# Performance work log

Hardware: AMD Instinct MI355X
Metric: run time of the kernel (lower is better)

## Reference

```python
import jax, jax.numpy as jnp
import numpy as np

NEG_SLOPE = 0.2


def gat_conv(h, src, dst, n_dst, W_src, W_dst, attn_l, attn_r, bias):
    # h: [N_src, F_in]; edges src->dst; dst nodes are a prefix of src nodes.
    H, D = attn_l.shape
    z_src = (h @ W_src).reshape(h.shape[0], H, D)          # [N_src, H, D]
    z_dst = (h[:n_dst] @ W_dst).reshape(n_dst, H, D)       # [N_dst, H, D]
    el = jnp.einsum('nhd,hd->nh', z_src, attn_l)           # [N_src, H]
    er = jnp.einsum('nhd,hd->nh', z_dst, attn_r)           # [N_dst, H]
    e = jax.nn.leaky_relu(el[src] + er[dst], NEG_SLOPE)    # [E, H]
    # numerically stable edge softmax over incoming edges of each dst node
    m = jax.ops.segment_max(e, dst, num_segments=n_dst)    # [N_dst, H]
    w = jnp.exp(e - m[dst])                                # [E, H]
    s = jax.ops.segment_sum(w, dst, num_segments=n_dst)    # [N_dst, H]
    alpha = w / s[dst]                                     # [E, H]
    msg = alpha[:, :, None] * z_src[src]                   # [E, H, D]
    out = jax.ops.segment_sum(msg, dst, num_segments=n_dst)
    return out + bias                                      # [N_dst, H, D]


def setup_inputs() -> dict:
    key = jax.random.key(0)
    ks = jax.random.split(key, 16)
    IN, HID, HEADS, NCLS = 256, 64, 4, 47
    N_SRC0, N_DST0, E0 = 200000, 50000, 500000
    N_DST1, E1 = 10000, 100000
    sc0 = 0.1
    inp = {
        'x': jax.random.normal(ks[0], (N_SRC0, IN), jnp.float32),
        'src0': jax.random.randint(ks[1], (E0,), 0, N_SRC0, jnp.int32),
        'dst0': jax.random.randint(ks[2], (E0,), 0, N_DST0, jnp.int32),
        'src1': jax.random.randint(ks[3], (E1,), 0, N_DST0, jnp.int32),
        'dst1': jax.random.randint(ks[4], (E1,), 0, N_DST1, jnp.int32),
        'num_dst0': N_DST0,
        'num_dst1': N_DST1,
        'W0_src': jax.random.normal(ks[5], (IN, HEADS * HID), jnp.float32) * sc0,
        'W0_dst': jax.random.normal(ks[6], (IN, HEADS * HID), jnp.float32) * sc0,
        'attn_l0': jax.random.normal(ks[7], (HEADS, HID), jnp.float32) * sc0,
        'attn_r0': jax.random.normal(ks[8], (HEADS, HID), jnp.float32) * sc0,
        'bias0': jnp.zeros((HEADS, HID), jnp.float32),
        'W1_src': jax.random.normal(ks[9], (HEADS * HID, HEADS * NCLS), jnp.float32) * sc0,
        'W1_dst': jax.random.normal(ks[10], (HEADS * HID, HEADS * NCLS), jnp.float32) * sc0,
        'attn_l1': jax.random.normal(ks[11], (HEADS, NCLS), jnp.float32) * sc0,
        'attn_r1': jax.random.normal(ks[12], (HEADS, NCLS), jnp.float32) * sc0,
        'bias1': jnp.zeros((HEADS, NCLS), jnp.float32),
    }
    return inp


def reference(x, src0, dst0, src1, dst1, num_dst0, num_dst1,
              W0_src, W0_dst, attn_l0, attn_r0, bias0,
              W1_src, W1_dst, attn_l1, attn_r1, bias1):
    # layer 0: GATConv + relu activation, flatten heads
    h = gat_conv(x, src0, dst0, num_dst0, W0_src, W0_dst, attn_l0, attn_r0, bias0)
    h = jax.nn.relu(h).reshape(num_dst0, -1)               # [N_dst0, H*HID]
    # layer 1: GATConv, no activation
    h = gat_conv(h, src1, dst1, num_dst1, W1_src, W1_dst, attn_l1, attn_r1, bias1)
    h = h.mean(axis=1)                                     # mean over heads -> [N_dst1, n_classes]
    return jax.nn.log_softmax(h, axis=-1)
```

## Files before the change

### kernel.cpp

```cpp
#include <hip/hip_runtime.h>
#include <math.h>

typedef _Float16 half8 __attribute__((ext_vector_type(8)));
typedef _Float16 half4 __attribute__((ext_vector_type(4)));
typedef float f32x16 __attribute__((ext_vector_type(16)));

constexpr int IN    = 256;
constexpr int NCLS  = 47;
constexpr int HD1   = 188;
constexpr float NEG_SLOPE = 0.2f;
constexpr int ND0 = 50000, ND1 = 10000;

static __device__ __forceinline__ float leaky(float x) {
    return x >= 0.f ? x : NEG_SLOPE * x;
}

__device__ __forceinline__ void gload16(const void* g, void* l) {
    __builtin_amdgcn_global_load_lds((const __attribute__((address_space(1))) void*)g,
                                     (__attribute__((address_space(3))) void*)l, 16, 0, 0);
}

__global__ __launch_bounds__(256) void prep_k(
        const float* __restrict__ W0s, const float* __restrict__ W1s,
        const float* __restrict__ W0d, const float* __restrict__ W1d,
        const float* __restrict__ ar0, const float* __restrict__ al1,
        const float* __restrict__ ar1,
        _Float16* __restrict__ B0t, _Float16* __restrict__ B1t,
        float* __restrict__ vr0T, float* __restrict__ vl1T, float* __restrict__ vr1T) {
    int b = blockIdx.x, t = threadIdx.x;
    if (b < 256) {
        int id = b * 256 + t;
        int n = id >> 8, k = id & 255;
        B0t[n * 256 + k] = (_Float16)W0s[(size_t)k * 256 + n];
    } else if (b < 448) {
        int id = (b - 256) * 256 + t;
        int n = id >> 8, k = id & 255;
        B1t[n * 256 + k] = (n < HD1) ? (_Float16)W1s[(size_t)k * HD1 + n] : (_Float16)0.f;
    } else if (b == 448) {
        for (int i = t; i < 1024; i += 256) {
            int h = i >> 8, k = i & 255;
            float s = 0.f;
            for (int d = 0; d < 64; ++d)
                s += W0d[(size_t)k * 256 + h * 64 + d] * ar0[h * 64 + d];
            vr0T[h * 256 + k] = s;
        }
    } else if (b == 449) {
        for (int i = t; i < 1024; i += 256) {
            int h = i >> 8, k = i & 255;
            float s = 0.f;
            for (int d = 0; d < NCLS; ++d)
                s += W1s[(size_t)k * HD1 + h * NCLS + d] * al1[h * NCLS + d];
            vl1T[h * 256 + k] = s;
        }
    } else {
        for (int i = t; i < 1024; i += 256) {
            int h = i >> 8, k = i & 255;
            float s = 0.f;
            for (int d = 0; d < NCLS; ++d)
                s += W1d[(size_t)k * HD1 + h * NCLS + d] * ar1[h * NCLS + d];
            vr1T[h * 256 + k] = s;
        }
    }
}

template <bool AHALF, int NWC, bool FEL>
__global__ __launch_bounds__(512, 4) void gemmk(const void* __restrict__ Av,
        const _Float16* __restrict__ Bt, _Float16* __restrict__ Z,
        const float* __restrict__ al, float* __restrict__ el, int M, int ntiles) {
    constexpr int ABYTES = AHALF ? 16 * 1040 : 32 * 1040;
    __shared__ __align__(16) char As[2][ABYTES];
    __shared__ float elp[2][8][32];
    __shared__ float alds[256];
    const int t = threadIdx.x, l = t & 63, w = t >> 6;
    const int l31 = l & 31, hi = l >> 5;
    const int G = gridDim.x;

    if (FEL && t < 256) alds[t] = al[t];

    half8 wk[16];
    {
        int wc = (w < NWC) ? w * 32 + l31 : 0;
        const _Float16* bp = Bt + (size_t)wc * 256 + hi * 8;
#pragma unroll
        for (int ks = 0; ks < 16; ++ks) wk[ks] = *(const half8*)(bp + ks * 16);
    }

    auto stage = [&](int buf, int tile) {
        if constexpr (AHALF) {
#pragma unroll
            for (int i = 0; i < 2; ++i) {
                int pr = w * 2 + i;
                int row = tile * 32 + pr * 2 + hi;
                if (row >= M) row = M - 1;
                gload16((const _Float16*)Av + (size_t)row * 256 + l31 * 8,
                        As[buf] + pr * 1040);
            }
        } else {
#pragma unroll
            for (int i = 0; i < 4; ++i) {
                int r = w * 4 + i;
                int row = tile * 32 + r;
                if (row >= M) row = M - 1;
                gload16((const float*)Av + (size_t)row * 256 + l * 4,
                        As[buf] + r * 1040);
            }
        }
    };

    int tile0 = blockIdx.x;
    stage(0, tile0);
    asm volatile("s_waitcnt vmcnt(0)" ::: "memory");
    __syncthreads();

    int buf = 0;
    for (int tile = tile0; tile < ntiles; tile += G) {
        int nxt = tile + G;
        if (nxt < ntiles) stage(buf ^ 1, nxt);

        if (w < NWC) {
            f32x16 acc;
#pragma unroll
            for (int e = 0; e < 16; ++e) acc[e] = 0.f;
#pragma unroll
            for (int ks = 0; ks < 16; ++ks) {
                half8 bf;
                if constexpr (AHALF) {
                    bf = *(const half8*)(As[buf] + (l31 >> 1) * 1040 + (l31 & 1) * 512
                                         + ks * 32 + hi * 16);
                } else {
                    const char* ab = As[buf] + l31 * 1040 + ks * 64 + hi * 32;
                    float4 f0 = *(const float4*)ab;
                    float4 f1 = *(const float4*)(ab + 16);
                    bf[0] = (_Float16)f0.x; bf[1] = (_Float16)f0.y;
                    bf[2] = (_Float16)f0.z; bf[3] = (_Float16)f0.w;
                    bf[4] = (_Float16)f1.x; bf[5] = (_Float16)f1.y;
                    bf[6] = (_Float16)f1.z; bf[7] = (_Float16)f1.w;
                }
                acc = __builtin_amdgcn_mfma_f32_32x32x16_f16(wk[ks], bf, acc, 0, 0, 0);
            }
            int xrow = tile * 32 + l31;
            if (xrow < M) {
#pragma unroll
                for (int g = 0; g < 4; ++g) {
                    half4 hv;
                    hv[0] = (_Float16)acc[g * 4 + 0]; hv[1] = (_Float16)acc[g * 4 + 1];
                    hv[2] = (_Float16)acc[g * 4 + 2]; hv[3] = (_Float16)acc[g * 4 + 3];
                    *(half4*)(Z + (size_t)xrow * (NWC * 32) + w * 32 + g * 8 + hi * 4) = hv;
                }
            }
            if constexpr (FEL) {
                float s = 0.f;
#pragma unroll
                for (int q = 0; q < 16; ++q)
                    s += acc[q] * alds[w * 32 + (q & 3) + 8 * (q >> 2) + 4 * hi];
                s += __shfl_xor(s, 32);
                if (hi == 0) elp[buf][w][l31] = s;
            }
        }
        asm volatile("s_waitcnt vmcnt(0)" ::: "memory");
        __syncthreads();
        if constexpr (FEL) {
            if (w < 4 && hi == 0) {
                int xrow = tile * 32 + l31;
                if (xrow < M)
                    el[(size_t)xrow * 4 + w] =
                        elp[buf][2 * w][l31] + elp[buf][2 * w + 1][l31];
            }
        }
        buf ^= 1;
    }
}

__global__ __launch_bounds__(256) void gemv_er_f32(const float* __restrict__ A,
        const float* __restrict__ vrT, float* __restrict__ er, int M) {
    int wv = threadIdx.x >> 6, lane = threadIdx.x & 63;
    int row = blockIdx.x * 4 + wv;
    if (row >= M) return;
    float4 xa = *(const float4*)(A + (size_t)row * IN + lane * 4);
    float s[4];
#pragma unroll
    for (int h = 0; h < 4; ++h) {
        float4 v = *(const float4*)(vrT + h * IN + lane * 4);
        s[h] = xa.x * v.x + xa.y * v.y + xa.z * v.z + xa.w * v.w;
    }
#pragma unroll
    for (int off = 32; off; off >>= 1)
#pragma unroll
        for (int h = 0; h < 4; ++h) s[h] += __shfl_xor(s[h], off);
    if (lane == 0) *(float4*)(er + (size_t)row * 4) = make_float4(s[0], s[1], s[2], s[3]);
}

__global__ __launch_bounds__(256) void gemv_lr_f16(const _Float16* __restrict__ A,
        const float* __restrict__ vlT, const float* __restrict__ vrT,
        float* __restrict__ el, float* __restrict__ er, int M, int Mr) {
    int wv = threadIdx.x >> 6, lane = threadIdx.x & 63;
    int row = blockIdx.x * 4 + wv;
    if (row >= M) return;
    half4 ah = *(const half4*)(A + (size_t)row * IN + lane * 4);
    float a0 = (float)ah[0], a1 = (float)ah[1], a2 = (float)ah[2], a3 = (float)ah[3];
    float sl[4], sr[4];
#pragma unroll
    for (int h = 0; h < 4; ++h) {
        float4 v = *(const float4*)(vlT + h * IN + lane * 4);
        sl[h] = a0 * v.x + a1 * v.y + a2 * v.z + a3 * v.w;
        float4 u = *(const float4*)(vrT + h * IN + lane * 4);
        sr[h] = a0 * u.x + a1 * u.y + a2 * u.z + a3 * u.w;
    }
#pragma unroll
    for (int off = 32; off; off >>= 1)
#pragma unroll
        for (int h = 0; h < 4; ++h) {
            sl[h] += __shfl_xor(sl[h], off);
            sr[h] += __shfl_xor(sr[h], off);
        }
    if (lane == 0) {
        *(float4*)(el + (size_t)row * 4) = make_float4(sl[0], sl[1], sl[2], sl[3]);
        if (row < Mr)
            *(float4*)(er + (size_t)row * 4) = make_float4(sr[0], sr[1], sr[2], sr[3]);
    }
}

__global__ void hist2_k(const int* __restrict__ dst0, int E0,
                        const int* __restrict__ dst1, int E1, int* __restrict__ counts) {
    int i = blockIdx.x * blockDim.x + threadIdx.x;
    if (i < E0) atomicAdd(&counts[dst0[i]], 1);
    else if (i < E0 + E1) atomicAdd(&counts[ND0 + dst1[i - E0]], 1);
}

__global__ __launch_bounds__(256) void scan1_k(const int* __restrict__ counts, int n,
                                               int* __restrict__ part) {
    __shared__ int ws[4];
    int i = blockIdx.x * 256 + threadIdx.x;
    int lane = threadIdx.x & 63, wv = threadIdx.x >> 6;
    int s = (i < n) ? counts[i] : 0;
#pragma unroll
    for (int off = 32; off; off >>= 1) s += __shfl_xor(s, off);
    if (lane == 0) ws[wv] = s;
    __syncthreads();
    if (threadIdx.x == 0) part[blockIdx.x] = ws[0] + ws[1] + ws[2] + ws[3];
}

__global__ __launch_bounds__(256) void scan2_k(int* __restrict__ part, int nb) {
    __shared__ int ws[4];
    int tid = threadIdx.x, lane = tid & 63, wv = tid >> 6;
    int v = (tid < nb) ? part[tid] : 0;
    int x = v;
#pragma unroll
    for (int off = 1; off < 64; off <<= 1) {
        int u = __shfl_up(x, off);
        if (lane >= off) x += u;
    }
    if (lane == 63) ws[wv] = x;
    __syncthreads();
    int base = 0;
    for (int k = 0; k < wv; ++k) base += ws[k];
    if (tid < nb) part[tid] = base + x - v;
}

__global__ __launch_bounds__(256) void scan3_k(const int* __restrict__ counts, int n,
        const int* __restrict__ part, int* __restrict__ offsets, int* __restrict__ cursor) {
    __shared__ int ws[4];
    int i = blockIdx.x * 256 + threadIdx.x;
    int lane = threadIdx.x & 63, wv = threadIdx.x >> 6;
    int v = (i < n) ? counts[i] : 0;
    int x = v;
#pragma unroll
    for (int off = 1; off < 64; off <<= 1) {
        int u = __shfl_up(x, off);
        if (lane >= off) x += u;
    }
    if (lane == 63) ws[wv] = x;
    __syncthreads();
    int base = part[blockIdx.x];
    for (int k = 0; k < wv; ++k) base += ws[k];
    int off_ = base + x - v;
    if (i < n) { offsets[i] = off_; cursor[i] = off_; }
    if (i == n - 1) offsets[n] = off_ + v;
}

__global__ void scatter2_k(const int* __restrict__ src0, const int* __restrict__ dst0, int E0,
                           const int* __restrict__ src1, const int* __restrict__ dst1, int E1,
                           int* __restrict__ cursor, int* __restrict__ ssrc) {
    int i = blockIdx.x * blockDim.x + threadIdx.x;
    if (i < E0) {
        int p = atomicAdd(&cursor[dst0[i]], 1);
        ssrc[p] = src0[i];
    } else if (i < E0 + E1) {
        int j = i - E0;
        int p = atomicAdd(&cursor[ND0 + dst1[j]], 1);
        ssrc[p] = src1[j];
    }
}

__global__ __launch_bounds__(256) void agg_l0(const int* __restrict__ ssrc,
        const int* __restrict__ offs, const float* __restrict__ el,
        const float* __restrict__ er, const _Float16* __restrict__ z,
        const float* __restrict__ bias, _Float16* __restrict__ h, int nd) {
    int wv = threadIdx.x >> 6, lane = threadIdx.x & 63;
    int d = blockIdx.x * 4 + wv;
    if (d >= nd) return;
    int head = lane >> 4;
    int beg = offs[d], end = offs[d + 1];
    float erh = er[(size_t)d * 4 + head];
    float ax = 0, ay = 0, az = 0, aw = 0, ssum = 0;
    for (int j0 = beg; j0 < end; j0 += 64) {
        int nn = min(64, end - j0);
        int myidx = (lane < nn) ? ssrc[j0 + lane] : 0;
        int j = 0;
        for (; j + 4 <= nn; j += 4) {
            int s0 = __shfl(myidx, j),     s1 = __shfl(myidx, j + 1);
            int s2 = __shfl(myidx, j + 2), s3 = __shfl(myidx, j + 3);
            float e0 = el[(size_t)s0 * 4 + head], e1 = el[(size_t)s1 * 4 + head];
            float e2 = el[(size_t)s2 * 4 + head], e3 = el[(size_t)s3 * 4 + head];
            half4 zv0 = *(const half4*)(z + (size_t)s0 * 256 + lane * 4);
            half4 zv1 = *(const half4*)(z + (size_t)s1 * 256 + lane * 4);
            half4 zv2 = *(const half4*)(z + (size_t)s2 * 256 + lane * 4);
            half4 zv3 = *(const half4*)(z + (size_t)s3 * 256 + lane * 4);
            float w0 = __expf(leaky(e0 + erh)), w1 = __expf(leaky(e1 + erh));
            float w2 = __expf(leaky(e2 + erh)), w3 = __expf(leaky(e3 + erh));
            ssum += (w0 + w1) + (w2 + w3);
            ax += w0 * (float)zv0[0] + w1 * (float)zv1[0] + w2 * (float)zv2[0] + w3 * (float)zv3[0];
            ay += w0 * (float)zv0[1] + w1 * (float)zv1[1] + w2 * (float)zv2[1] + w3 * (float)zv3[1];
            az += w0 * (float)zv0[2] + w1 * (float)zv1[2] + w2 * (float)zv2[2] + w3 * (float)zv3[2];
            aw += w0 * (float)zv0[3] + w1 * (float)zv1[3] + w2 * (float)zv2[3] + w3 * (float)zv3[3];
        }
        for (; j < nn; ++j) {
            int s = __shfl(myidx, j);
            float e = el[(size_t)s * 4 + head] + erh;
            float wgt = __expf(leaky(e));
            ssum += wgt;
            half4 zv = *(const half4*)(z + (size_t)s * 256 + lane * 4);
            ax += wgt * (float)zv[0]; ay += wgt * (float)zv[1];
            az += wgt * (float)zv[2]; aw += wgt * (float)zv[3];
        }
    }
    float inv = ssum > 0.f ? 1.f / ssum : 0.f;
    const float* b = bias + lane * 4;
    half4 o;
    o[0] = (_Float16)fmaxf(ax * inv + b[0], 0.f);
    o[1] = (_Float16)fmaxf(ay * inv + b[1], 0.f);
    o[2] = (_Float16)fmaxf(az * inv + b[2], 0.f);
    o[3] = (_Float16)fmaxf(aw * inv + b[3], 0.f);
    *(half4*)(h + (size_t)d * 256 + lane * 4) = o;
}

__global__ __launch_bounds__(256) void agg_l1f(const int* __restrict__ ssrc,
        const int* __restrict__ offs, const float* __restrict__ el,
        const float* __restrict__ er, const _Float16* __restrict__ z,
        const float* __restrict__ bias, float* __restrict__ y, int nd) {
    __shared__ float ro[4][192];
    int wv = threadIdx.x >> 6, lane = threadIdx.x & 63;
    int d = blockIdx.x * 4 + wv;
    if (d >= nd) return;
    int beg = offs[ND0 + d], end = offs[ND0 + d + 1];
    float4 er4 = *(const float4*)(er + (size_t)d * 4);
    const int f0 = lane, f1 = lane + 64, f2 = lane + 128;
    const int h0 = f0 / NCLS, h1 = f1 / NCLS;
    const bool has2 = f2 < HD1;
    const int h2 = has2 ? f2 / NCLS : 3;
    float a0 = 0, a1 = 0, a2 = 0;
    float s0 = 0, s1 = 0, s2 = 0, s3 = 0;
    for (int j0 = beg; j0 < end; j0 += 64) {
        int nn = min(64, end - j0);
        int myidx = (lane < nn) ? ssrc[j0 + lane] : 0;
        int j = 0;
        for (; j + 2 <= nn; j += 2) {
            int sa_ = __shfl(myidx, j), sb_ = __shfl(myidx, j + 1);
            float4 ea = *(const float4*)(el + (size_t)sa_ * 4);
            float4 eb = *(const float4*)(el + (size_t)sb_ * 4);
            const _Float16* za = z + (size_t)sa_ * 192;
            const _Float16* zb = z + (size_t)sb_ * 192;
            float za0 = (float)za[f0], za1 = (float)za[f1], za2 = has2 ? (float)za[f2] : 0.f;
            float zb0 = (float)zb[f0], zb1 = (float)zb[f1], zb2 = has2 ? (float)zb[f2] : 0.f;
            float wa0 = __expf(leaky(ea.x + er4.x)), wa1 = __expf(leaky(ea.y + er4.y));
            float wa2 = __expf(leaky(ea.z + er4.z)), wa3 = __expf(leaky(ea.w + er4.w));
            float wb0 = __expf(leaky(eb.x + er4.x)), wb1 = __expf(leaky(eb.y + er4.y));
            float wb2 = __expf(leaky(eb.z + er4.z)), wb3 = __expf(leaky(eb.w + er4.w));
            s0 += wa0 + wb0; s1 += wa1 + wb1; s2 += wa2 + wb2; s3 += wa3 + wb3;
            a0 += (h0 == 0 ? wa0 : h0 == 1 ? wa1 : h0 == 2 ? wa2 : wa3) * za0
                + (h0 == 0 ? wb0 : h0 == 1 ? wb1 : h0 == 2 ? wb2 : wb3) * zb0;
            a1 += (h1 == 0 ? wa0 : h1 == 1 ? wa1 : h1 == 2 ? wa2 : wa3) * za1
                + (h1 == 0 ? wb0 : h1 == 1 ? wb1 : h1 == 2 ? wb2 : wb3) * zb1;
            if (has2)
                a2 += (h2 == 0 ? wa0 : h2 == 1 ? wa1 : h2 == 2 ? wa2 : wa3) * za2
                    + (h2 == 0 ? wb0 : h2 == 1 ? wb1 : h2 == 2 ? wb2 : wb3) * zb2;
        }
        for (; j < nn; ++j) {
            int s = __shfl(myidx, j);
            float4 e4 = *(const float4*)(el + (size_t)s * 4);
            float w0 = __expf(leaky(e4.x + er4.x));
            float w1 = __expf(leaky(e4.y + er4.y));
            float w2 = __expf(leaky(e4.z + er4.z));
            float w3 = __expf(leaky(e4.w + er4.w));
            s0 += w0; s1 += w1; s2 += w2; s3 += w3;
            const _Float16* zr = z + (size_t)s * 192;
            a0 += (h0 == 0 ? w0 : h0 == 1 ? w1 : h0 == 2 ? w2 : w3) * (float)zr[f0];
            a1 += (h1 == 0 ? w0 : h1 == 1 ? w1 : h1 == 2 ? w2 : w3) * (float)zr[f1];
            if (has2) a2 += (h2 == 0 ? w0 : h2 == 1 ? w1 : h2 == 2 ? w2 : w3) * (float)zr[f2];
        }
    }
    float sa = h0 == 0 ? s0 : h0 == 1 ? s1 : h0 == 2 ? s2 : s3;
    float sb = h1 == 0 ? s0 : h1 == 1 ? s1 : h1 == 2 ? s2 : s3;
    float sc = h2 == 0 ? s0 : h2 == 1 ? s1 : h2 == 2 ? s2 : s3;
    ro[wv][f0] = a0 * (sa > 0.f ? 1.f / sa : 0.f) + bias[f0];
    ro[wv][f1] = a1 * (sb > 0.f ? 1.f / sb : 0.f) + bias[f1];
    if (has2) ro[wv][f2] = a2 * (sc > 0.f ? 1.f / sc : 0.f) + bias[f2];
    asm volatile("s_waitcnt lgkmcnt(0)" ::: "memory");
    __builtin_amdgcn_sched_barrier(0);
    float vv = 0.f, v = -INFINITY;
    if (lane < NCLS) {
        vv = 0.25f * (ro[wv][lane] + ro[wv][lane + NCLS] +
                      ro[wv][lane + 2 * NCLS] + ro[wv][lane + 3 * NCLS]);
        v = vv;
    }
    float mx = v;
#pragma unroll
    for (int off = 32; off; off >>= 1) mx = fmaxf(mx, __shfl_xor(mx, off));
    float pp = (lane < NCLS) ? __expf(vv - mx) : 0.f;
    float sum = pp;
#pragma unroll
    for (int off = 32; off; off >>= 1) sum += __shfl_xor(sum, off);
    if (lane < NCLS) y[(size_t)d * NCLS + lane] = vv - mx - logf(sum);
}

extern "C" void kernel_launch(void* const* d_in, const int* in_sizes, int n_in,
                              void* d_out, int out_size, void* d_ws, size_t ws_size,
                              hipStream_t stream) {
    const float* x    = (const float*)d_in[0];
    const int*   src0 = (const int*)d_in[1];
    const int*   dst0 = (const int*)d_in[2];
    const int*   src1 = (const int*)d_in[3];
    const int*   dst1 = (const int*)d_in[4];
    const float* W0s  = (const float*)d_in[7];
    const float* W0d  = (const float*)d_in[8];
    const float* al0  = (const float*)d_in[9];
    const float* ar0  = (const float*)d_in[10];
    const float* b0   = (const float*)d_in[11];
    const float* W1s  = (const float*)d_in[12];
    const float* W1d  = (const float*)d_in[13];
    const float* al1  = (const float*)d_in[14];
    const float* ar1  = (const float*)d_in[15];
    const float* b1   = (const float*)d_in[16];
    const int E0 = in_sizes[1], E1 = in_sizes[3];
    const int NS0 = in_sizes[0] / IN;

    char* p = (char*)d_ws;
    auto take = [&](size_t bytes) {
        char* r = p;
        p += (bytes + 255) & ~(size_t)255;
        return r;
    };
    _Float16* z0   = (_Float16*)take((size_t)NS0 * 256 * 2);
    _Float16* h    = (_Float16*)take((size_t)ND0 * 256 * 2);
    _Float16* z1   = (_Float16*)take((size_t)ND0 * 192 * 2);
    float*    el0  = (float*)take((size_t)NS0 * 4 * 4);
    float*    er0  = (float*)take((size_t)ND0 * 4 * 4);
    float*    el1  = (float*)take((size_t)ND0 * 4 * 4);
    float*    er1  = (float*)take((size_t)ND1 * 4 * 4);
    _Float16* B0t  = (_Float16*)take((size_t)256 * 256 * 2);
    _Float16* B1t  = (_Float16*)take((size_t)192 * 256 * 2);
    float*    vr0T = (float*)take(4 * 256 * 4);
    float*    vl1T = (float*)take(4 * 256 * 4);
    float*    vr1T = (float*)take(4 * 256 * 4);
    const int NDT = ND0 + ND1;
    int* counts = (int*)take((size_t)NDT * 4);
    int* offs   = (int*)take((size_t)(NDT + 1) * 4);
    int* cur    = (int*)take((size_t)NDT * 4);
    int* ss     = (int*)take((size_t)(E0 + E1) * 4);
    int* part   = (int*)take(256 * 4);

    const int NB = (NDT + 255) / 256;
    const int NT0 = (NS0 + 31) / 32, NT1 = (ND0 + 31) / 32;
    const int G0 = NT0 < 512 ? NT0 : 512, G1 = NT1 < 512 ? NT1 : 512;

    hipMemsetAsync(counts, 0, (size_t)NDT * 4, stream);

    prep_k<<<451, 256, 0, stream>>>(W0s, W1s, W0d, W1d, ar0, al1, ar1,
                                    B0t, B1t, vr0T, vl1T, vr1T);
    hist2_k<<<(E0 + E1 + 255) / 256, 256, 0, stream>>>(dst0, E0, dst1, E1, counts);
    scan1_k<<<NB, 256, 0, stream>>>(counts, NDT, part);
    scan2_k<<<1, 256, 0, stream>>>(part, NB);
    scan3_k<<<NB, 256, 0, stream>>>(counts, NDT, part, offs, cur);
    scatter2_k<<<(E0 + E1 + 255) / 256, 256, 0, stream>>>(src0, dst0, E0, src1, dst1, E1,
                                                          cur, ss);

    gemmk<false, 8, true><<<G0, 512, 0, stream>>>(
        (const void*)x, B0t, z0, al0, el0, NS0, NT0);
    gemv_er_f32<<<(ND0 + 3) / 4, 256, 0, stream>>>(x, vr0T, er0, ND0);
    agg_l0<<<(ND0 + 3) / 4, 256, 0, stream>>>(ss, offs, el0, er0, z0, b0, h, ND0);

    gemmk<true, 6, false><<<G1, 512, 0, stream>>>(
        (const void*)h, B1t, z1, nullptr, nullptr, ND0, NT1);
    gemv_lr_f16<<<(ND0 + 3) / 4, 256, 0, stream>>>(h, vl1T, vr1T, el1, er1, ND0, ND1);
    agg_l1f<<<(ND1 + 3) / 4, 256, 0, stream>>>(ss, offs, el1, er1, z1, b1,
                                               (float*)d_out, ND1);
}
```

Baseline: 321.9 us.

## Stage GEMM A tiles through registers as fp16 with swizzled LDS layout

Replaces the direct global-to-LDS loads with register prefetch of the next tile. The fp32 input is converted to fp16 before it is written into a smaller, XOR-swizzled LDS buffer, so MFMA operand reads become single conflict-free half8 loads. The el epilogue is restructured to run after one barrier per iteration instead of two, with a final flush after the loop. This cuts LDS footprint and conversion work in the inner loop, at the cost of extra registers to hold the prefetched payload.

```diff
diff --git a/kernel.cpp b/kernel.cpp
--- a/kernel.cpp
+++ b/kernel.cpp
@@ -13,11 +13,6 @@
 
 static __device__ __forceinline__ float leaky(float x) {
     return x >= 0.f ? x : NEG_SLOPE * x;
-}
-
-__device__ __forceinline__ void gload16(const void* g, void* l) {
-    __builtin_amdgcn_global_load_lds((const __attribute__((address_space(1))) void*)g,
-                                     (__attribute__((address_space(3))) void*)l, 16, 0, 0);
 }
 
 __global__ __launch_bounds__(256) void prep_k(
@@ -67,8 +62,7 @@
 __global__ __launch_bounds__(512, 4) void gemmk(const void* __restrict__ Av,
         const _Float16* __restrict__ Bt, _Float16* __restrict__ Z,
         const float* __restrict__ al, float* __restrict__ el, int M, int ntiles) {
-    constexpr int ABYTES = AHALF ? 16 * 1040 : 32 * 1040;
-    __shared__ __align__(16) char As[2][ABYTES];
+    __shared__ __align__(16) char As[2][32 * 576];
     __shared__ float elp[2][8][32];
     __shared__ float alds[256];
     const int t = threadIdx.x, l = t & 63, w = t >> 6;
@@ -85,57 +79,59 @@
         for (int ks = 0; ks < 16; ++ks) wk[ks] = *(const half8*)(bp + ks * 16);
     }
 
-    auto stage = [&](int buf, int tile) {
-        if constexpr (AHALF) {
-#pragma unroll
-            for (int i = 0; i < 2; ++i) {
-                int pr = w * 2 + i;
-                int row = tile * 32 + pr * 2 + hi;
-                if (row >= M) row = M - 1;
-                gload16((const _Float16*)Av + (size_t)row * 256 + l31 * 8,
-                        As[buf] + pr * 1040);
+    float4 payf[4];
+    half4  payh[4];
+
+    auto issue = [&](int tile) {
+#pragma unroll
+        for (int i = 0; i < 4; ++i) {
+            int row = tile * 32 + w * 4 + i;
+            if (row >= M) row = M - 1;
+            if constexpr (AHALF)
+                payh[i] = *(const half4*)((const _Float16*)Av + (size_t)row * 256 + l * 4);
+            else
+                payf[i] = *(const float4*)((const float*)Av + (size_t)row * 256 + l * 4);
+        }
+        __builtin_amdgcn_sched_barrier(0);
+    };
+
+    auto write_lds = [&](int b) {
+#pragma unroll
+        for (int i = 0; i < 4; ++i) {
+            int rr = w * 4 + i;
+            half4 hv;
+            if constexpr (AHALF) {
+                hv = payh[i];
+            } else {
+                hv[0] = (_Float16)payf[i].x; hv[1] = (_Float16)payf[i].y;
+                hv[2] = (_Float16)payf[i].z; hv[3] = (_Float16)payf[i].w;
             }
-        } else {
-#pragma unroll
-            for (int i = 0; i < 4; ++i) {
-                int r = w * 4 + i;
-                int row = tile * 32 + r;
-                if (row >= M) row = M - 1;
-                gload16((const float*)Av + (size_t)row * 256 + l * 4,
-                        As[buf] + r * 1040);
+            *(half4*)(As[b] + rr * 576 + ((((l >> 1) ^ rr) & 31) << 4) + (l & 1) * 8) = hv;
+        }
+    };
+
+    int tile0 = blockIdx.x;
+    issue(tile0);
+    int b = 0, prev = -1;
+    for (int tile = tile0; tile < ntiles; tile += G) {
+        write_lds(b);
+        if (tile + G < ntiles) issue(tile + G);
+        __syncthreads();
+        if constexpr (FEL) {
+            if (prev >= 0 && w < 4 && hi == 0) {
+                int xr = prev * 32 + l31;
+                if (xr < M)
+                    el[(size_t)xr * 4 + w] = elp[b ^ 1][2 * w][l31] + elp[b ^ 1][2 * w + 1][l31];
             }
         }
-    };
-
-    int tile0 = blockIdx.x;
-    stage(0, tile0);
-    asm volatile("s_waitcnt vmcnt(0)" ::: "memory");
-    __syncthreads();
-
-    int buf = 0;
-    for (int tile = tile0; tile < ntiles; tile += G) {
-        int nxt = tile + G;
-        if (nxt < ntiles) stage(buf ^ 1, nxt);
-
         if (w < NWC) {
             f32x16 acc;
 #pragma unroll
             for (int e = 0; e < 16; ++e) acc[e] = 0.f;
 #pragma unroll
             for (int ks = 0; ks < 16; ++ks) {
-                half8 bf;
-                if constexpr (AHALF) {
-                    bf = *(const half8*)(As[buf] + (l31 >> 1) * 1040 + (l31 & 1) * 512
-                                         + ks * 32 + hi * 16);
-                } else {
-                    const char* ab = As[buf] + l31 * 1040 + ks * 64 + hi * 32;
-                    float4 f0 = *(const float4*)ab;
-                    float4 f1 = *(const float4*)(ab + 16);
-                    bf[0] = (_Float16)f0.x; bf[1] = (_Float16)f0.y;
-                    bf[2] = (_Float16)f0.z; bf[3] = (_Float16)f0.w;
-                    bf[4] = (_Float16)f1.x; bf[5] = (_Float16)f1.y;
-                    bf[6] = (_Float16)f1.z; bf[7] = (_Float16)f1.w;
-                }
+                const char* pa = As[b] + l31 * 576 + ((((ks * 2 + hi) ^ l31) & 31) << 4);
+                half8 bf = *(const half8*)pa;
                 acc = __builtin_amdgcn_mfma_f32_32x32x16_f16(wk[ks], bf, acc, 0, 0, 0);
             }
             int xrow = tile * 32 + l31;
@@ -154,20 +150,19 @@
                 for (int q = 0; q < 16; ++q)
                     s += acc[q] * alds[w * 32 + (q & 3) + 8 * (q >> 2) + 4 * hi];
                 s += __shfl_xor(s, 32);
-                if (hi == 0) elp[buf][w][l31] = s;
+                if (hi == 0) elp[b][w][l31] = s;
             }
         }
-        asm volatile("s_waitcnt vmcnt(0)" ::: "memory");
+        prev = tile;
+        b ^= 1;
+    }
+    if constexpr (FEL) {
         __syncthreads();
-        if constexpr (FEL) {
-            if (w < 4 && hi == 0) {
-                int xrow = tile * 32 + l31;
-                if (xrow < M)
-                    el[(size_t)xrow * 4 + w] =
-                        elp[buf][2 * w][l31] + elp[buf][2 * w + 1][l31];
-            }
-        }
-        buf ^= 1;
+        if (prev >= 0 && w < 4 && hi == 0) {
+            int xr = prev * 32 + l31;
+            if (xr < M)
+                el[(size_t)xr * 4 + w] = elp[b ^ 1][2 * w][l31] + elp[b ^ 1][2 * w + 1][l31];
+        }
     }
 }
 
```

Result: slower. 328.5 us (+2.1%).

## Pre-convert x to fp16 with fused el/er GEMV and 4-stage swizzled GEMM pipeline

Applied to the files above, without the earlier changes.

A new cvt_lr kernel reads x once, writes an fp16 copy, and computes el0 and er0 through precomputed W0s·attn_l and W0d·attn_r vectors. This replaces the el epilogue inside the GEMM and the separate er GEMV. The GEMM is rewritten as gemmd: fp16 input only, a 4-deep LDS ring buffer with a partial vmcnt wait, and XOR-swizzled LDS addressing in place of padded rows. The trade-off is an extra fp16 write and read of x (about 100MB of traffic) in exchange for a simpler, deeper-pipelined MFMA loop with half the A-tile staging bytes.

```diff
diff --git a/kernel.cpp b/kernel.cpp
--- a/kernel.cpp
+++ b/kernel.cpp
@@ -23,10 +23,11 @@
 __global__ __launch_bounds__(256) void prep_k(
         const float* __restrict__ W0s, const float* __restrict__ W1s,
         const float* __restrict__ W0d, const float* __restrict__ W1d,
-        const float* __restrict__ ar0, const float* __restrict__ al1,
-        const float* __restrict__ ar1,
+        const float* __restrict__ al0, const float* __restrict__ ar0,
+        const float* __restrict__ al1, const float* __restrict__ ar1,
         _Float16* __restrict__ B0t, _Float16* __restrict__ B1t,
-        float* __restrict__ vr0T, float* __restrict__ vl1T, float* __restrict__ vr1T) {
+        float* __restrict__ vl0T, float* __restrict__ vr0T,
+        float* __restrict__ vl1T, float* __restrict__ vr1T) {
     int b = blockIdx.x, t = threadIdx.x;
     if (b < 256) {
         int id = b * 256 + t;
@@ -48,6 +49,14 @@
         for (int i = t; i < 1024; i += 256) {
             int h = i >> 8, k = i & 255;
             float s = 0.f;
+            for (int d = 0; d < 64; ++d)
+                s += W0s[(size_t)k * 256 + h * 64 + d] * al0[h * 64 + d];
+            vl0T[h * 256 + k] = s;
+        }
+    } else if (b == 450) {
+        for (int i = t; i < 1024; i += 256) {
+            int h = i >> 8, k = i & 255;
+            float s = 0.f;
             for (int d = 0; d < NCLS; ++d)
                 s += W1s[(size_t)k * HD1 + h * NCLS + d] * al1[h * NCLS + d];
             vl1T[h * 256 + k] = s;
@@ -63,19 +72,49 @@
     }
 }
 
-template <bool AHALF, int NWC, bool FEL>
-__global__ __launch_bounds__(512, 4) void gemmk(const void* __restrict__ Av,
-        const _Float16* __restrict__ Bt, _Float16* __restrict__ Z,
-        const float* __restrict__ al, float* __restrict__ el, int M, int ntiles) {
-    constexpr int ABYTES = AHALF ? 16 * 1040 : 32 * 1040;
-    __shared__ __align__(16) char As[2][ABYTES];
-    __shared__ float elp[2][8][32];
-    __shared__ float alds[256];
+__global__ __launch_bounds__(256) void cvt_lr(const float* __restrict__ x,
+        const float* __restrict__ vlT, const float* __restrict__ vrT,
+        _Float16* __restrict__ xh, float* __restrict__ el, float* __restrict__ er,
+        int M, int Mr) {
+    int wv = threadIdx.x >> 6, lane = threadIdx.x & 63;
+    int row = blockIdx.x * 4 + wv;
+    if (row >= M) return;
+    float4 xa = *(const float4*)(x + (size_t)row * IN + lane * 4);
+    half4 hv;
+    hv[0] = (_Float16)xa.x; hv[1] = (_Float16)xa.y;
+    hv[2] = (_Float16)xa.z; hv[3] = (_Float16)xa.w;
+    *(half4*)(xh + (size_t)row * IN + lane * 4) = hv;
+    float sl[4], sr[4];
+    bool do_r = row < Mr;
+#pragma unroll
+    for (int h = 0; h < 4; ++h) {
+        float4 v = *(const float4*)(vlT + h * IN + lane * 4);
+        sl[h] = xa.x * v.x + xa.y * v.y + xa.z * v.z + xa.w * v.w;
+        float4 u = *(const float4*)(vrT + h * IN + lane * 4);
+        sr[h] = xa.x * u.x + xa.y * u.y + xa.z * u.z + xa.w * u.w;
+    }
+#pragma unroll
+    for (int off = 32; off; off >>= 1)
+#pragma unroll
+        for (int h = 0; h < 4; ++h) {
+            sl[h] += __shfl_xor(sl[h], off);
+            sr[h] += __shfl_xor(sr[h], off);
+        }
+    if (lane == 0) {
+        *(float4*)(el + (size_t)row * 4) = make_float4(sl[0], sl[1], sl[2], sl[3]);
+        if (do_r)
+            *(float4*)(er + (size_t)row * 4) = make_float4(sr[0], sr[1], sr[2], sr[3]);
+    }
+}
+
+template <int NWC>
+__global__ __launch_bounds__(512, 4) void gemmd(const _Float16* __restrict__ Ah,
+        const _Float16* __restrict__ Bt, _Float16* __restrict__ Z, int M, int ntiles) {
+    __shared__ __align__(16) char As[4][16384];
     const int t = threadIdx.x, l = t & 63, w = t >> 6;
     const int l31 = l & 31, hi = l >> 5;
     const int G = gridDim.x;
-
-    if (FEL && t < 256) alds[t] = al[t];
+    const int tile0 = blockIdx.x;
 
     half8 wk[16];
     {
@@ -85,60 +124,38 @@
         for (int ks = 0; ks < 16; ++ks) wk[ks] = *(const half8*)(bp + ks * 16);
     }
 
-    auto stage = [&](int buf, int tile) {
-        if constexpr (AHALF) {
-#pragma unroll
-            for (int i = 0; i < 2; ++i) {
-                int pr = w * 2 + i;
-                int row = tile * 32 + pr * 2 + hi;
-                if (row >= M) row = M - 1;
-                gload16((const _Float16*)Av + (size_t)row * 256 + l31 * 8,
-                        As[buf] + pr * 1040);
-            }
-        } else {
-#pragma unroll
-            for (int i = 0; i < 4; ++i) {
-                int r = w * 4 + i;
-                int row = tile * 32 + r;
-                if (row >= M) row = M - 1;
-                gload16((const float*)Av + (size_t)row * 256 + l * 4,
-                        As[buf] + r * 1040);
-            }
+    auto stage = [&](int it) {
+        int tile = tile0 + it * G;
+        if (tile >= ntiles) return;
+        char* dst = As[it & 3];
+#pragma unroll
+        for (int i = 0; i < 2; ++i) {
+            int c = i * 512 + t;
+            int r = c >> 5, s = c & 31;
+            int row = tile * 32 + r; if (row >= M) row = M - 1;
+            gload16(Ah + (size_t)row * 256 + ((s ^ r) << 3), dst + c * 16);
         }
     };
 
-    int tile0 = blockIdx.x;
-    stage(0, tile0);
-    asm volatile("s_waitcnt vmcnt(0)" ::: "memory");
-    __syncthreads();
-
-    int buf = 0;
-    for (int tile = tile0; tile < ntiles; tile += G) {
-        int nxt = tile + G;
-        if (nxt < ntiles) stage(buf ^ 1, nxt);
-
+    int nit = 0;
+    if (tile0 < ntiles) nit = (ntiles - 1 - tile0) / G + 1;
+
+    stage(0); stage(1); stage(2);
+    for (int it = 0; it < nit; ++it) {
+        asm volatile("s_waitcnt vmcnt(4)" ::: "memory");
+        __syncthreads();
+        stage(it + 3);
         if (w < NWC) {
+            const char* buf = As[it & 3];
             f32x16 acc;
 #pragma unroll
             for (int e = 0; e < 16; ++e) acc[e] = 0.f;
 #pragma unroll
             for (int ks = 0; ks < 16; ++ks) {
-                half8 bf;
-                if constexpr (AHALF) {
-                    bf = *(const half8*)(As[buf] + (l31 >> 1) * 1040 + (l31 & 1) * 512
-                                         + ks * 32 + hi * 16);
-                } else {
-                    const char* ab = As[buf] + l31 * 1040 + ks * 64 + hi * 32;
-                    float4 f0 = *(const float4*)ab;
-                    float4 f1 = *(const float4*)(ab + 16);
-                    bf[0] = (_Float16)f0.x; bf[1] = (_Float16)f0.y;
-                    bf[2] = (_Float16)f0.z; bf[3] = (_Float16)f0.w;
-                    bf[4] = (_Float16)f1.x; bf[5] = (_Float16)f1.y;
-                    bf[6] = (_Float16)f1.z; bf[7] = (_Float16)f1.w;
-                }
+                half8 bf = *(const half8*)(buf + l31 * 512 + (((2 * ks + hi) ^ l31) << 4));
                 acc = __builtin_amdgcn_mfma_f32_32x32x16_f16(wk[ks], bf, acc, 0, 0, 0);
             }
-            int xrow = tile * 32 + l31;
+            int xrow = (tile0 + it * G) * 32 + l31;
             if (xrow < M) {
 #pragma unroll
                 for (int g = 0; g < 4; ++g) {
@@ -148,46 +165,8 @@
                     *(half4*)(Z + (size_t)xrow * (NWC * 32) + w * 32 + g * 8 + hi * 4) = hv;
                 }
             }
-            if constexpr (FEL) {
-                float s = 0.f;
-#pragma unroll
-                for (int q = 0; q < 16; ++q)
-                    s += acc[q] * alds[w * 32 + (q & 3) + 8 * (q >> 2) + 4 * hi];
-                s += __shfl_xor(s, 32);
-                if (hi == 0) elp[buf][w][l31] = s;
-            }
-        }
-        asm volatile("s_waitcnt vmcnt(0)" ::: "memory");
-        __syncthreads();
-        if constexpr (FEL) {
-            if (w < 4 && hi == 0) {
-                int xrow = tile * 32 + l31;
-                if (xrow < M)
-                    el[(size_t)xrow * 4 + w] =
-                        elp[buf][2 * w][l31] + elp[buf][2 * w + 1][l31];
-            }
-        }
-        buf ^= 1;
-    }
-}
-
-__global__ __launch_bounds__(256) void gemv_er_f32(const float* __restrict__ A,
-        const float* __restrict__ vrT, float* __restrict__ er, int M) {
-    int wv = threadIdx.x >> 6, lane = threadIdx.x & 63;
-    int row = blockIdx.x * 4 + wv;
-    if (row >= M) return;
-    float4 xa = *(const float4*)(A + (size_t)row * IN + lane * 4);
-    float s[4];
-#pragma unroll
-    for (int h = 0; h < 4; ++h) {
-        float4 v = *(const float4*)(vrT + h * IN + lane * 4);
-        s[h] = xa.x * v.x + xa.y * v.y + xa.z * v.z + xa.w * v.w;
-    }
-#pragma unroll
-    for (int off = 32; off; off >>= 1)
-#pragma unroll
-        for (int h = 0; h < 4; ++h) s[h] += __shfl_xor(s[h], off);
-    if (lane == 0) *(float4*)(er + (size_t)row * 4) = make_float4(s[0], s[1], s[2], s[3]);
+        }
+    }
 }
 
 __global__ __launch_bounds__(256) void gemv_lr_f16(const _Float16* __restrict__ A,
@@ -450,6 +429,7 @@
         p += (bytes + 255) & ~(size_t)255;
         return r;
     };
+    _Float16* xh   = (_Float16*)take((size_t)NS0 * 256 * 2);
     _Float16* z0   = (_Float16*)take((size_t)NS0 * 256 * 2);
     _Float16* h    = (_Float16*)take((size_t)ND0 * 256 * 2);
     _Float16* z1   = (_Float16*)take((size_t)ND0 * 192 * 2);
@@ -459,6 +439,7 @@
     float*    er1  = (float*)take((size_t)ND1 * 4 * 4);
     _Float16* B0t  = (_Float16*)take((size_t)256 * 256 * 2);
     _Float16* B1t  = (_Float16*)take((size_t)192 * 256 * 2);
+    float*    vl0T = (float*)take(4 * 256 * 4);
     float*    vr0T = (float*)take(4 * 256 * 4);
     float*    vl1T = (float*)take(4 * 256 * 4);
     float*    vr1T = (float*)take(4 * 256 * 4);
@@ -475,8 +456,8 @@
 
     hipMemsetAsync(counts, 0, (size_t)NDT * 4, stream);
 
-    prep_k<<<451, 256, 0, stream>>>(W0s, W1s, W0d, W1d, ar0, al1, ar1,
-                                    B0t, B1t, vr0T, vl1T, vr1T);
+    prep_k<<<452, 256, 0, stream>>>(W0s, W1s, W0d, W1d, al0, ar0, al1, ar1,
+                                    B0t, B1t, vl0T, vr0T, vl1T, vr1T);
     hist2_k<<<(E0 + E1 + 255) / 256, 256, 0, stream>>>(dst0, E0, dst1, E1, counts);
     scan1_k<<<NB, 256, 0, stream>>>(counts, NDT, part);
     scan2_k<<<1, 256, 0, stream>>>(part, NB);
@@ -484,13 +465,11 @@
     scatter2_k<<<(E0 + E1 + 255) / 256, 256, 0, stream>>>(src0, dst0, E0, src1, dst1, E1,
                                                           cur, ss);
 
-    gemmk<false, 8, true><<<G0, 512, 0, stream>>>(
-        (const void*)x, B0t, z0, al0, el0, NS0, NT0);
-    gemv_er_f32<<<(ND0 + 3) / 4, 256, 0, stream>>>(x, vr0T, er0, ND0);
+    cvt_lr<<<(NS0 + 3) / 4, 256, 0, stream>>>(x, vl0T, vr0T, xh, el0, er0, NS0, ND0);
+    gemmd<8><<<G0, 512, 0, stream>>>(xh, B0t, z0, NS0, NT0);
     agg_l0<<<(ND0 + 3) / 4, 256, 0, stream>>>(ss, offs, el0, er0, z0, b0, h, ND0);
 
-    gemmk<true, 6, false><<<G1, 512, 0, stream>>>(
-        (const void*)h, B1t, z1, nullptr, nullptr, ND0, NT1);
+    gemmd<6><<<G1, 512, 0, stream>>>(h, B1t, z1, ND0, NT1);
     gemv_lr_f16<<<(ND0 + 3) / 4, 256, 0, stream>>>(h, vl1T, vr1T, el1, er1, ND0, ND1);
     agg_l1f<<<(ND1 + 3) / 4, 256, 0, stream>>>(ss, offs, el1, er1, z1, b1,
                                                (float*)d_out, ND1);
```

Measured after the change: 363.2 us. +12.9%, slower.
